# Kernel tuning notes

Measured on AMD Instinct MI355X. Metric: run time of the kernel, lower is better.

Reference implementation:

```python
import jax, jax.numpy as jnp
import numpy as np

# Module config (matches init_kwargs)
RADIUS = 1
N_POINTS = 8
NUM_BINS = 8
DENSITY = True
LBP_MAX = 2 ** N_POINTS - 1  # 255


def _circle_offsets(radius, n_points):
    # skimage local_binary_pattern sampling coordinates:
    # rr = -radius*sin(2*pi*i/P), cc = radius*cos(2*pi*i/P)
    offs = []
    for i in range(n_points):
        ang = 2.0 * np.pi * i / n_points
        dy = -radius * np.sin(ang)
        dx = radius * np.cos(ang)
        # skimage snaps near-integer coords to exact integers (eps rounding)
        if abs(dy - round(dy)) < 1e-8:
            dy = float(round(dy))
        if abs(dx - round(dx)) < 1e-8:
            dx = float(round(dx))
        offs.append((dy, dx))
    return offs


def _bilinear_shift(xp, pad, dy, dx, H, W):
    # Bilinear sample of every pixel's neighbor at constant offset (dy, dx),
    # zero padding outside the image (skimage uses constant-0 border mode).
    fy, fx = int(np.floor(dy)), int(np.floor(dx))
    ty, tx = dy - fy, dx - fx

    def sl(oy, ox):
        return xp[..., pad + oy:pad + oy + H, pad + ox:pad + ox + W]

    return ((1.0 - ty) * (1.0 - tx) * sl(fy, fx)
            + (1.0 - ty) * tx * sl(fy, fx + 1)
            + ty * (1.0 - tx) * sl(fy + 1, fx)
            + ty * tx * sl(fy + 1, fx + 1))


def _lbp_codes(x):
    # x: (B, C, H, W) -> integer-valued LBP codes (B, C, H, W), method='default'
    B, C, H, W = x.shape
    pad = int(np.ceil(RADIUS)) + 1
    xp = jnp.pad(x, ((0, 0), (0, 0), (pad, pad), (pad, pad)))
    code = jnp.zeros(x.shape, dtype=jnp.float32)
    for i, (dy, dx) in enumerate(_circle_offsets(RADIUS, N_POINTS)):
        nb = _bilinear_shift(xp, pad, dy, dx, H, W)
        bit = (nb - x >= 0).astype(jnp.float32)
        code = code + bit * float(2 ** i)
    return code


def _histogram(codes):
    # np.histogram(bins=NUM_BINS, range=(0, LBP_MAX), density=True) per channel
    B, C, H, W = codes.shape
    width = LBP_MAX / NUM_BINS
    idx = jnp.clip((codes * (1.0 / width)).astype(jnp.int32), 0, NUM_BINS - 1)
    idx_flat = idx.reshape(B * C, H * W)
    counts = jax.vmap(
        lambda ix: jnp.zeros((NUM_BINS,), jnp.float32).at[ix].add(1.0)
    )(idx_flat)  # (B*C, NUM_BINS)
    if DENSITY:
        counts = counts / (float(H * W) * width)
    return counts.reshape(B, C, NUM_BINS)


def setup_inputs() -> dict:
    key = jax.random.key(0)
    x = jax.random.normal(key, (32, 3, 512, 512), dtype=jnp.float32)
    return {"x": x}


def reference(x):
    codes = _lbp_codes(x)               # (B, C, H, W)
    hist = _histogram(codes)            # (B, C, NUM_BINS)
    return hist.reshape(hist.shape[0], -1).astype(jnp.float32)  # (B, C*NUM_BINS)
```

## Files before the change

### kernel.cpp

```cpp
#include <hip/hip_runtime.h>

#define W 512
#define H 512
#define CH_PIX (W * H)

__device__ __forceinline__ float2 lr_for(float4 v, float hk, int half, int lane) {
    const float up = __shfl_up(v.w, 1, 64);
    const float dn = __shfl_down(v.x, 1, 64);
    const float eL = half ? hk : 0.0f;
    const float eR = half ? 0.0f : hk;
    float2 r;
    r.x = (lane == 0)  ? eL : up;
    r.y = (lane == 63) ? eR : dn;
    return r;
}

__global__ __launch_bounds__(256) void lbp_main_k(const float* __restrict__ x,
                                                  unsigned int* __restrict__ ws) {
    const int chan = blockIdx.x;
    const int band = blockIdx.y;
    const int tid  = threadIdx.x;
    const int wave  = tid >> 6;
    const int lane  = tid & 63;
    const int strip = wave >> 1;
    const int half  = wave & 1;

    __shared__ unsigned int h[8 * 64];
    for (int i = tid; i < 512; i += 256) h[i] = 0u;
    __syncthreads();

    constexpr double Sd = 0.7071067811865476;
    constexpr double Td = 1.0 - Sd;
    const float wSS = (float)(Sd * Sd);
    const float wST = (float)(Sd * Td);
    const float wTT = (float)(Td * Td);

    const int colbase = half * 256 + lane * 4;
    const int haloCol = half ? 255 : 256;
    const size_t cb   = (size_t)chan * CH_PIX;

    unsigned long long c64 = 0ull;

    auto rowpix = [&](const float4& m4, float mL, float mR,
                      const float4& d4, float dL, float dR) {
        const float cs[4]  = {m4.x, m4.y, m4.z, m4.w};
        const float es[4]  = {m4.y, m4.z, m4.w, mR};
        const float wsA[4] = {mL,   m4.x, m4.y, m4.z};
        const float ss[4]  = {d4.x, d4.y, d4.z, d4.w};
        const float sws[4] = {dL,   d4.x, d4.y, d4.z};
        const float ses[4] = {d4.y, d4.z, d4.w, dR};
        #pragma unroll
        for (int i = 0; i < 4; ++i) {
            const float c  = cs[i];
            const float tc = wTT * c;
            const float ts = wST * ss[i];
            const float nb5 = ((wST * wsA[i] + tc) + wSS * sws[i]) + ts;
            const float nb7 = ((tc + wST * es[i]) + ts) + wSS * ses[i];
            const unsigned int amt = (nb5   >= c ? 8u  : 0u)
                                   + (ss[i] >= c ? 16u : 0u)
                                   + (nb7   >= c ? 32u : 0u);
            c64 += 1ull << amt;
        }
    };

    if (band < 16) {
        const int y0 = band * 32 + strip * 16;
        const int nr = (y0 == 496) ? 15 : 16;

        float4 r4[17];
        #pragma unroll
        for (int k = 0; k < 17; ++k) {
            int yy = y0 + k; yy = yy > 511 ? 511 : yy;
            r4[k] = *(const float4*)(x + cb + yy * W + colbase);
        }
        float hvAll = 0.0f;
        if (lane < 17) {
            int yy = y0 + lane; yy = yy > 511 ? 511 : yy;
            hvAll = x[cb + yy * W + haloCol];
        }

        float4 m4  = r4[0];
        float2 mlr = lr_for(m4, __shfl(hvAll, 0, 64), half, lane);

        #pragma unroll
        for (int k = 0; k < 16; ++k) {
            if (k < nr) {
                const float4 d4  = r4[k + 1];
                const float2 dlr = lr_for(d4, __shfl(hvAll, k + 1, 64), half, lane);
                rowpix(m4, mlr.x, mlr.y, d4, dlr.x, dlr.y);
                m4 = d4; mlr = dlr;
            }
        }
    } else if (strip == 0) {
        const float4 m4 = *(const float4*)(x + cb + 511 * W + colbase);
        float hvAll = 0.0f;
        if (lane == 0) hvAll = x[cb + 511 * W + haloCol];
        const float2 mlr = lr_for(m4, __shfl(hvAll, 0, 64), half, lane);
        const float mL = mlr.x, mR = mlr.y;

        const float cs[4]  = {m4.x, m4.y, m4.z, m4.w};
        const float es[4]  = {m4.y, m4.z, m4.w, mR};
        const float wsA[4] = {mL,   m4.x, m4.y, m4.z};
        #pragma unroll
        for (int i = 0; i < 4; ++i) {
            const float c  = cs[i];
            const float tc = wTT * c;
            const float nb5 = ((wST * wsA[i] + tc) + wSS * 0.0f) + wST * 0.0f;
            const float nb7 = ((tc + wST * es[i]) + wST * 0.0f) + wSS * 0.0f;
            const unsigned int amt = (nb5  >= c ? 8u  : 0u)
                                   + (0.0f >= c ? 16u : 0u)
                                   + (nb7  >= c ? 32u : 0u);
            c64 += 1ull << amt;
        }
    }

    const unsigned int lo = (unsigned int)c64;
    const unsigned int hi = (unsigned int)(c64 >> 32);
    #pragma unroll
    for (int b = 0; b < 4; ++b) {
        atomicAdd(&h[(b       << 6) + lane], (lo >> (b * 8)) & 0xffu);
        atomicAdd(&h[((b + 4) << 6) + lane], (hi >> (b * 8)) & 0xffu);
    }
    __syncthreads();

    if (tid < 8) {
        unsigned int s = 0;
        #pragma unroll
        for (int l = 0; l < 64; ++l) s += h[(tid << 6) + l];
        ws[(chan * 17 + band) * 8 + tid] = s;
    }
}

__global__ __launch_bounds__(64) void finalize_k(const unsigned int* __restrict__ ws,
                                                 float* __restrict__ out) {
    const int gid = blockIdx.x * 64 + threadIdx.x;
    if (gid < 768) {
        const int chan = gid >> 3, bin = gid & 7;
        unsigned int s = 0;
        #pragma unroll
        for (int b = 0; b < 17; ++b) s += ws[(chan * 17 + b) * 8 + bin];
        out[gid] = (float)s / 8355840.0f;
    }
}

extern "C" void kernel_launch(void* const* d_in, const int* in_sizes, int n_in,
                              void* d_out, int out_size, void* d_ws, size_t ws_size,
                              hipStream_t stream) {
    const float* x = (const float*)d_in[0];
    unsigned int* wsp = (unsigned int*)d_ws;
    float* out = (float*)d_out;

    dim3 grid(96, 17);
    lbp_main_k<<<grid, 256, 0, stream>>>(x, wsp);
    finalize_k<<<12, 64, 0, stream>>>(wsp, out);
}
```

Measured before the change: 27.00 us.

## Fold last row into final strip, stage row loads in groups, add occupancy hint

The separate 17th band that handled only image row 511 is removed. The last strip now processes that row itself by feeding a zeroed south neighbour, so the grid shrinks to 96x16 and finalize sums 16 partials. Row loads are issued in staged groups interleaved with computation instead of all upfront, which aims to cut register pressure and overlap memory with ALU work. Launch bounds request 5 waves per SIMD, and address math moves to 32-bit ints. The occupancy cap could cause spills if the register budget gets tight.

After: 33.66 us. 1.25x slower.

```diff
diff --git a/kernel.cpp b/kernel.cpp
--- a/kernel.cpp
+++ b/kernel.cpp
@@ -15,8 +15,8 @@
     return r;
 }
 
-__global__ __launch_bounds__(256) void lbp_main_k(const float* __restrict__ x,
-                                                  unsigned int* __restrict__ ws) {
+__global__ __launch_bounds__(256, 5) void lbp_main_k(const float* __restrict__ x,
+                                                     unsigned int* __restrict__ ws) {
     const int chan = blockIdx.x;
     const int band = blockIdx.y;
     const int tid  = threadIdx.x;
@@ -35,11 +35,28 @@
     const float wST = (float)(Sd * Td);
     const float wTT = (float)(Td * Td);
 
-    const int colbase = half * 256 + lane * 4;
+    const int colbase = half * 256 + (lane << 2);
     const int haloCol = half ? 255 : 256;
-    const size_t cb   = (size_t)chan * CH_PIX;
+    const int cb   = chan * CH_PIX;
+    const int y0   = band * 32 + strip * 16;
+    const bool lastStrip = (y0 == 496);
+    const int base = cb + y0 * W + colbase;
 
     unsigned long long c64 = 0ull;
+    float4 buf[17];
+
+    #pragma unroll
+    for (int k = 0; k < 5; ++k) buf[k] = *(const float4*)(x + base + k * W);
+
+    float hvAll = 0.0f;
+    {
+        int yy = y0 + lane;
+        yy = yy > 511 ? 511 : yy;
+        if (lane < 17) hvAll = x[cb + yy * W + haloCol];
+    }
+
+    #pragma unroll
+    for (int k = 5; k < 9; ++k) buf[k] = *(const float4*)(x + base + k * W);
 
     auto rowpix = [&](const float4& m4, float mL, float mR,
                       const float4& d4, float dL, float dR) {
@@ -63,56 +80,33 @@
         }
     };
 
-    if (band < 16) {
-        const int y0 = band * 32 + strip * 16;
-        const int nr = (y0 == 496) ? 15 : 16;
+    float4 m4  = buf[0];
+    float2 mlr = lr_for(m4, __shfl(hvAll, 0, 64), half, lane);
 
-        float4 r4[17];
-        #pragma unroll
-        for (int k = 0; k < 17; ++k) {
-            int yy = y0 + k; yy = yy > 511 ? 511 : yy;
-            r4[k] = *(const float4*)(x + cb + yy * W + colbase);
-        }
-        float hvAll = 0.0f;
-        if (lane < 17) {
-            int yy = y0 + lane; yy = yy > 511 ? 511 : yy;
-            hvAll = x[cb + yy * W + haloCol];
-        }
+    #define ROWSTEP(k)                                                       \
+    {                                                                        \
+        float4 d4 = buf[(k) + 1];                                            \
+        float dhk = __shfl(hvAll, (k) + 1, 64);                              \
+        if (lastStrip && (k) == 15) {                                        \
+            d4.x = 0.0f; d4.y = 0.0f; d4.z = 0.0f; d4.w = 0.0f; dhk = 0.0f;  \
+        }                                                                    \
+        const float2 dlr = lr_for(d4, dhk, half, lane);                      \
+        rowpix(m4, mlr.x, mlr.y, d4, dlr.x, dlr.y);                          \
+        m4 = d4; mlr = dlr;                                                  \
+    }
 
-        float4 m4  = r4[0];
-        float2 mlr = lr_for(m4, __shfl(hvAll, 0, 64), half, lane);
-
-        #pragma unroll
-        for (int k = 0; k < 16; ++k) {
-            if (k < nr) {
-                const float4 d4  = r4[k + 1];
-                const float2 dlr = lr_for(d4, __shfl(hvAll, k + 1, 64), half, lane);
-                rowpix(m4, mlr.x, mlr.y, d4, dlr.x, dlr.y);
-                m4 = d4; mlr = dlr;
-            }
-        }
-    } else if (strip == 0) {
-        const float4 m4 = *(const float4*)(x + cb + 511 * W + colbase);
-        float hvAll = 0.0f;
-        if (lane == 0) hvAll = x[cb + 511 * W + haloCol];
-        const float2 mlr = lr_for(m4, __shfl(hvAll, 0, 64), half, lane);
-        const float mL = mlr.x, mR = mlr.y;
-
-        const float cs[4]  = {m4.x, m4.y, m4.z, m4.w};
-        const float es[4]  = {m4.y, m4.z, m4.w, mR};
-        const float wsA[4] = {mL,   m4.x, m4.y, m4.z};
-        #pragma unroll
-        for (int i = 0; i < 4; ++i) {
-            const float c  = cs[i];
-            const float tc = wTT * c;
-            const float nb5 = ((wST * wsA[i] + tc) + wSS * 0.0f) + wST * 0.0f;
-            const float nb7 = ((tc + wST * es[i]) + wST * 0.0f) + wSS * 0.0f;
-            const unsigned int amt = (nb5  >= c ? 8u  : 0u)
-                                   + (0.0f >= c ? 16u : 0u)
-                                   + (nb7  >= c ? 32u : 0u);
-            c64 += 1ull << amt;
-        }
+    ROWSTEP(0) ROWSTEP(1) ROWSTEP(2) ROWSTEP(3)
+    #pragma unroll
+    for (int k = 9; k < 13; ++k) buf[k] = *(const float4*)(x + base + k * W);
+    ROWSTEP(4) ROWSTEP(5) ROWSTEP(6) ROWSTEP(7)
+    #pragma unroll
+    for (int k = 13; k < 17; ++k) {
+        const int kk = (k == 16 && lastStrip) ? 15 : k;
+        buf[k] = *(const float4*)(x + base + kk * W);
     }
+    ROWSTEP(8) ROWSTEP(9) ROWSTEP(10) ROWSTEP(11)
+    ROWSTEP(12) ROWSTEP(13) ROWSTEP(14) ROWSTEP(15)
+    #undef ROWSTEP
 
     const unsigned int lo = (unsigned int)c64;
     const unsigned int hi = (unsigned int)(c64 >> 32);
@@ -127,7 +121,7 @@
         unsigned int s = 0;
         #pragma unroll
         for (int l = 0; l < 64; ++l) s += h[(tid << 6) + l];
-        ws[(chan * 17 + band) * 8 + tid] = s;
+        ws[(chan * 16 + band) * 8 + tid] = s;
     }
 }
 
@@ -138,7 +132,7 @@
         const int chan = gid >> 3, bin = gid & 7;
         unsigned int s = 0;
         #pragma unroll
-        for (int b = 0; b < 17; ++b) s += ws[(chan * 17 + b) * 8 + bin];
+        for (int b = 0; b < 16; ++b) s += ws[(chan * 16 + b) * 8 + bin];
         out[gid] = (float)s / 8355840.0f;
     }
 }
@@ -150,7 +144,7 @@
     unsigned int* wsp = (unsigned int*)d_ws;
     float* out = (float*)d_out;
 
-    dim3 grid(96, 17);
+    dim3 grid(96, 16);
     lbp_main_k<<<grid, 256, 0, stream>>>(x, wsp);
     finalize_k<<<12, 64, 0, stream>>>(wsp, out);
 }
```
